# Kernel tuning notes

Hardware: AMD Instinct MI355X
Metric: run time of the kernel (lower is better)

## Reference

```python
import jax, jax.numpy as jnp
import numpy as np

W1 = 7          # half window
W2 = 2 * W1 + 1 # window size = 15
H = 4           # num heads
DH = 64         # head dim
DO = H * DH     # 256


def setup_inputs() -> dict:
    key = jax.random.key(0)
    ks = jax.random.split(key, 7)
    B, T, D = 2, 4096, 768
    s = 1.0 / np.sqrt(D).astype(np.float32)
    inputs = jax.random.normal(ks[0], (B, T, D), dtype=jnp.float32)
    Wq = jax.random.normal(ks[1], (DO, D), dtype=jnp.float32) * s
    bq = jax.random.normal(ks[2], (DO,), dtype=jnp.float32) * s
    Wv = jax.random.normal(ks[3], (DO, D), dtype=jnp.float32) * s
    bv = jax.random.normal(ks[4], (DO,), dtype=jnp.float32) * s
    pos_emb = jax.random.normal(ks[5], (W2, D), dtype=jnp.float32)
    return {"inputs": inputs, "Wq": Wq, "bq": bq, "Wv": Wv, "bv": bv, "pos_emb": pos_emb}


def reference(inputs, Wq, bq, Wv, bv, pos_emb):
    # Faithful to the torch module: k uses the *query* projection (source bug),
    # no softmax, no 1/sqrt(d) scaling.
    B, T, D = inputs.shape
    pad = jnp.pad(inputs, ((0, 0), (W1, W1), (0, 0)))  # [B, T+2*W1, D]
    # Project once on the padded sequence, then gather windows (linear ops
    # commute with the window gather; position bias added post-projection).
    q_pad = pad @ Wq.T + bq            # [B, T+2*W1, DO]
    v_pad = pad @ Wv.T + bv            # [B, T+2*W1, DO]
    pos_q = pos_emb @ Wq.T             # [W2, DO]  (query(window+pos) = query(window)+pos@Wq^T)
    pos_v = pos_emb @ Wv.T             # [W2, DO]
    idx = jnp.arange(T)[:, None] + jnp.arange(W2)[None, :]  # [T, W2]
    k = q_pad[:, idx] + pos_q          # [B, T, W2, DO]
    v = v_pad[:, idx] + pos_v          # [B, T, W2, DO]
    q = inputs @ Wq.T + bq             # [B, T, DO]
    qh = q.reshape(B, T, H, DH)
    kh = k.reshape(B, T, W2, H, DH)
    vh = v.reshape(B, T, W2, H, DH)
    scores = jnp.einsum('bthd,btwhd->bthw', qh, kh)   # [B, T, H, W2] (no softmax)
    ctx = jnp.einsum('bthw,btwhd->bthd', scores, vh)  # [B, T, H, DH]
    return ctx.reshape(B, T, DO)
```

## Files before the change

### kernel.cpp

```cpp
#include <hip/hip_runtime.h>

#define TPC   4110
#define MROWS 8220
#define MTOT  8235
#define MPAD  8320
#define KD    768
#define NSTR  4

typedef __attribute__((ext_vector_type(8))) short short8;
typedef __attribute__((ext_vector_type(4))) float f32x4;

#define LOAD_LDS16(gp, lp)                                                   \
  __builtin_amdgcn_global_load_lds(                                          \
      (const __attribute__((address_space(1))) void*)(gp),                   \
      (__attribute__((address_space(3))) void*)(lp), 16, 0, 0)

__device__ inline unsigned bfr(float x) {
  unsigned u = __float_as_uint(x);
  return (u + 0x7FFFu + ((u >> 16) & 1u)) >> 16;
}
__device__ inline unsigned pack2(float a, float b) {
  return bfr(a) | (bfr(b) << 16);
}

__global__ __launch_bounds__(256) void cast_pass(
    const float* __restrict__ inp, const float* __restrict__ Wq,
    const float* __restrict__ Wv, const float* __restrict__ pos,
    ushort* __restrict__ Abf, ushort* __restrict__ Wbf) {
  const int ACH = MPAD * 96;
  int gid = blockIdx.x * 256 + threadIdx.x;
  const float* src = nullptr;
  ushort* dst;
  if (gid < ACH) {
    int row = gid / 96, c = (gid - row * 96) * 8;
    dst = Abf + (size_t)row * KD + c;
    if (row < MROWS) {
      int b = row / TPC, tp = row - b * TPC, t = tp - 7;
      if (t >= 0 && t < 4096) src = inp + ((size_t)b * 4096 + t) * KD + c;
    } else if (row < MTOT) {
      src = pos + (size_t)(row - MROWS) * KD + c;
    }
  } else {
    int wid = gid - ACH;
    if (wid >= 512 * 96) return;
    int row = wid / 96, c = (wid - row * 96) * 8;
    dst = Wbf + (size_t)row * KD + c;
    src = (row < 256) ? Wq + (size_t)row * KD + c
                      : Wv + (size_t)(row - 256) * KD + c;
  }
  uint4 o;
  if (src) {
    float4 f0 = *(const float4*)src;
    float4 f1 = *(const float4*)(src + 4);
    o.x = pack2(f0.x, f0.y); o.y = pack2(f0.z, f0.w);
    o.z = pack2(f1.x, f1.y); o.w = pack2(f1.z, f1.w);
  } else {
    o.x = o.y = o.z = o.w = 0u;
  }
  *(uint4*)dst = o;
}

__global__ __launch_bounds__(256) void proj_gemm_bf16(
    const ushort* __restrict__ Abf, const ushort* __restrict__ Wbf,
    const float* __restrict__ bq, const float* __restrict__ bv,
    float* __restrict__ q_out, float* __restrict__ v_out) {
  __shared__ ushort Alds[128 * 32];
  __shared__ ushort Blds[128 * 32];
  const int tid = threadIdx.x;
  const int wave = tid >> 6, lane = tid & 63;
  const int nstrip = blockIdx.x;
  const int m0 = blockIdx.y * 128;
  const int wm = wave & 1, wn = wave >> 1;
  const int fr = lane & 15, quad = lane >> 4;

  f32x4 acc[4][4];
  #pragma unroll
  for (int i = 0; i < 4; i++)
    #pragma unroll
    for (int j = 0; j < 4; j++) acc[i][j] = 0.0f;

  const int r0 = tid >> 2, g0 = (tid & 3) * 8;
  const size_t a_base0 = (size_t)(m0 + r0) * KD + g0;
  const size_t a_base1 = (size_t)(m0 + 64 + r0) * KD + g0;
  const size_t b_base0 = (size_t)(nstrip * 128 + r0) * KD + g0;
  const size_t b_base1 = (size_t)(nstrip * 128 + 64 + r0) * KD + g0;
  ushort* aw0 = Alds + (size_t)(wave * 64) * 8;
  ushort* aw1 = Alds + (size_t)(256 + wave * 64) * 8;
  ushort* bw0 = Blds + (size_t)(wave * 64) * 8;
  ushort* bw1 = Blds + (size_t)(256 + wave * 64) * 8;

  for (int k0 = 0; k0 < KD; k0 += 32) {
    LOAD_LDS16(Abf + a_base0 + k0, aw0);
    LOAD_LDS16(Abf + a_base1 + k0, aw1);
    LOAD_LDS16(Wbf + b_base0 + k0, bw0);
    LOAD_LDS16(Wbf + b_base1 + k0, bw1);
    __syncthreads();
    short8 a[4], b[4];
    #pragma unroll
    for (int i = 0; i < 4; i++)
      a[i] = *(const short8*)(Alds + (wm * 64 + i * 16 + fr) * 32 + quad * 8);
    #pragma unroll
    for (int j = 0; j < 4; j++)
      b[j] = *(const short8*)(Blds + (wn * 64 + j * 16 + fr) * 32 + quad * 8);
    #pragma unroll
    for (int i = 0; i < 4; i++)
      #pragma unroll
      for (int j = 0; j < 4; j++)
        acc[i][j] = __builtin_amdgcn_mfma_f32_16x16x32_bf16(a[i], b[j],
                                                            acc[i][j], 0, 0, 0);
    __syncthreads();
  }

  const float* bias = (nstrip < 2) ? bq : bv;
  float* dst = (nstrip < 2) ? q_out : v_out;
  const int colb = (nstrip & 1) * 128;
  #pragma unroll
  for (int j = 0; j < 4; j++) {
    int col = colb + wn * 64 + j * 16 + fr;
    float bj = bias[col];
    #pragma unroll
    for (int i = 0; i < 4; i++) {
      int mbase = m0 + wm * 64 + i * 16 + quad * 4;
      #pragma unroll
      for (int r = 0; r < 4; r++) {
        int m = mbase + r;
        if (m < MTOT) {
          float v = acc[i][j][r] + (m < MROWS ? bj : 0.0f);
          dst[(size_t)m * 256 + col] = v;
        }
      }
    }
  }
}

__global__ __launch_bounds__(256) void win_attn2(
    const float* __restrict__ q_out, const float* __restrict__ v_out,
    float* __restrict__ out) {
  __shared__ __align__(16) float ks[78][68];
  __shared__ __align__(16) float vs[78][68];
  __shared__ __align__(16) float pq[15][68];
  __shared__ __align__(16) float pv[15][68];
  const int tid = threadIdx.x;
  const int bh = blockIdx.x >> 6, tile = blockIdx.x & 63;
  const int b = bh >> 2, h = bh & 3;
  const int t0 = tile * 64;
  const int colbase = h * 64;

  for (int idx = tid; idx < 78 * 16; idx += 256) {
    int row = idx >> 4, c4 = (idx & 15) * 4;
    size_t go = ((size_t)(b * TPC + t0 + row)) * 256 + colbase + c4;
    *(float4*)&ks[row][c4] = *(const float4*)(q_out + go);
    *(float4*)&vs[row][c4] = *(const float4*)(v_out + go);
  }
  if (tid < 15 * 16) {
    int row = tid >> 4, c4 = (tid & 15) * 4;
    size_t go = ((size_t)(MROWS + row)) * 256 + colbase + c4;
    *(float4*)&pq[row][c4] = *(const float4*)(q_out + go);
    *(float4*)&pv[row][c4] = *(const float4*)(v_out + go);
  }
  __syncthreads();

  const int tl = tid >> 2, qtr = tid & 3, d0 = qtr * 16;
  float4 qv[4];
  #pragma unroll
  for (int c = 0; c < 4; c++) qv[c] = *(float4*)&ks[tl + 7][d0 + c * 4];
  float4 ctx[4];
  #pragma unroll
  for (int c = 0; c < 4; c++) ctx[c] = make_float4(0.f, 0.f, 0.f, 0.f);

  #pragma unroll
  for (int w = 0; w < 15; w++) {
    float p = 0.f;
    #pragma unroll
    for (int c = 0; c < 4; c++) {
      float4 kk = *(float4*)&ks[tl + w][d0 + c * 4];
      float4 pp = *(float4*)&pq[w][d0 + c * 4];
      p += qv[c].x * (kk.x + pp.x) + qv[c].y * (kk.y + pp.y) +
           qv[c].z * (kk.z + pp.z) + qv[c].w * (kk.w + pp.w);
    }
    p += __shfl_xor(p, 1, 64);
    p += __shfl_xor(p, 2, 64);
    #pragma unroll
    for (int c = 0; c < 4; c++) {
      float4 vv = *(float4*)&vs[tl + w][d0 + c * 4];
      float4 pp = *(float4*)&pv[w][d0 + c * 4];
      ctx[c].x += p * (vv.x + pp.x);
      ctx[c].y += p * (vv.y + pp.y);
      ctx[c].z += p * (vv.z + pp.z);
      ctx[c].w += p * (vv.w + pp.w);
    }
  }
  size_t oo = ((size_t)(b * 4096 + t0 + tl)) * 256 + colbase + d0;
  #pragma unroll
  for (int c = 0; c < 4; c++) *(float4*)(out + oo + c * 4) = ctx[c];
}

extern "C" void kernel_launch(void* const* d_in, const int* in_sizes, int n_in,
                              void* d_out, int out_size, void* d_ws,
                              size_t ws_size, hipStream_t stream) {
  const float* inp = (const float*)d_in[0];
  const float* Wq  = (const float*)d_in[1];
  const float* bq  = (const float*)d_in[2];
  const float* Wv  = (const float*)d_in[3];
  const float* bv  = (const float*)d_in[4];
  const float* pos = (const float*)d_in[5];
  float* out = (float*)d_out;

  char* ws = (char*)d_ws;
  ushort* Abf  = (ushort*)ws;
  ushort* Wbf  = (ushort*)(ws + 12779520);
  float*  q_out = (float*)(ws + 13565952);
  float*  v_out = (float*)(ws + 22085632);

  const int cast_chunks = MPAD * 96 + 512 * 96;
  hipLaunchKernelGGL(cast_pass, dim3(cast_chunks / 256), dim3(256), 0, stream,
                     inp, Wq, Wv, pos, Abf, Wbf);
  hipLaunchKernelGGL(proj_gemm_bf16, dim3(NSTR, MPAD / 128), dim3(256), 0,
                     stream, Abf, Wbf, bq, bv, q_out, v_out);
  hipLaunchKernelGGL(win_attn2, dim3(2 * 4 * 64), dim3(256), 0, stream,
                     q_out, v_out, out);
}
```

Baseline: 119.5 us.

## Fuse bf16 cast into projection GEMM and store head-major Q/V slabs

Removes the separate cast kernel. The projection GEMM now loads fp32 inputs and weights directly, converts them to bf16 in registers and stores them to LDS, prefetching the next K tile into registers. The M tile shrinks from 128 to 64 with an occupancy hint, and Q/V outputs are written in a [b,h,t,d] layout with the position projections in separate buffers, so the attention kernel reads contiguous slabs. This trades the intermediate bf16 round trip and one launch for double the fp32 weight reads (redundant across M tiles), scattered epilogue stores, and register-staged loads instead of direct-to-LDS loads.

```diff
diff --git a/kernel.cpp b/kernel.cpp
--- a/kernel.cpp
+++ b/kernel.cpp
@@ -3,17 +3,10 @@
 #define TPC   4110
 #define MROWS 8220
 #define MTOT  8235
-#define MPAD  8320
 #define KD    768
-#define NSTR  4
 
 typedef __attribute__((ext_vector_type(8))) short short8;
 typedef __attribute__((ext_vector_type(4))) float f32x4;
-
-#define LOAD_LDS16(gp, lp)                                                   \
-  __builtin_amdgcn_global_load_lds(                                          \
-      (const __attribute__((address_space(1))) void*)(gp),                   \
-      (__attribute__((address_space(3))) void*)(lp), 16, 0, 0)
 
 __device__ inline unsigned bfr(float x) {
   unsigned u = __float_as_uint(x);
@@ -23,118 +16,123 @@
   return bfr(a) | (bfr(b) << 16);
 }
 
-__global__ __launch_bounds__(256) void cast_pass(
+__global__ __launch_bounds__(256, 3) void proj_fused(
     const float* __restrict__ inp, const float* __restrict__ Wq,
-    const float* __restrict__ Wv, const float* __restrict__ pos,
-    ushort* __restrict__ Abf, ushort* __restrict__ Wbf) {
-  const int ACH = MPAD * 96;
-  int gid = blockIdx.x * 256 + threadIdx.x;
-  const float* src = nullptr;
-  ushort* dst;
-  if (gid < ACH) {
-    int row = gid / 96, c = (gid - row * 96) * 8;
-    dst = Abf + (size_t)row * KD + c;
-    if (row < MROWS) {
-      int b = row / TPC, tp = row - b * TPC, t = tp - 7;
-      if (t >= 0 && t < 4096) src = inp + ((size_t)b * 4096 + t) * KD + c;
-    } else if (row < MTOT) {
-      src = pos + (size_t)(row - MROWS) * KD + c;
-    }
-  } else {
-    int wid = gid - ACH;
-    if (wid >= 512 * 96) return;
-    int row = wid / 96, c = (wid - row * 96) * 8;
-    dst = Wbf + (size_t)row * KD + c;
-    src = (row < 256) ? Wq + (size_t)row * KD + c
-                      : Wv + (size_t)(row - 256) * KD + c;
-  }
-  uint4 o;
-  if (src) {
-    float4 f0 = *(const float4*)src;
-    float4 f1 = *(const float4*)(src + 4);
-    o.x = pack2(f0.x, f0.y); o.y = pack2(f0.z, f0.w);
-    o.z = pack2(f1.x, f1.y); o.w = pack2(f1.z, f1.w);
-  } else {
-    o.x = o.y = o.z = o.w = 0u;
-  }
-  *(uint4*)dst = o;
-}
-
-__global__ __launch_bounds__(256) void proj_gemm_bf16(
-    const ushort* __restrict__ Abf, const ushort* __restrict__ Wbf,
-    const float* __restrict__ bq, const float* __restrict__ bv,
-    float* __restrict__ q_out, float* __restrict__ v_out) {
-  __shared__ ushort Alds[128 * 32];
-  __shared__ ushort Blds[128 * 32];
+    const float* __restrict__ bq, const float* __restrict__ Wv,
+    const float* __restrict__ bv, const float* __restrict__ pos,
+    float* __restrict__ q_out, float* __restrict__ v_out,
+    float* __restrict__ pos_q, float* __restrict__ pos_v) {
+  __shared__ ushort Al[64 * 32];
+  __shared__ ushort Bl[128 * 32];
   const int tid = threadIdx.x;
   const int wave = tid >> 6, lane = tid & 63;
-  const int nstrip = blockIdx.x;
-  const int m0 = blockIdx.y * 128;
+  const int ns = blockIdx.x;
+  const int m0 = blockIdx.y * 64;
   const int wm = wave & 1, wn = wave >> 1;
   const int fr = lane & 15, quad = lane >> 4;
 
-  f32x4 acc[4][4];
-  #pragma unroll
-  for (int i = 0; i < 4; i++)
+  const int sr = tid >> 2;
+  const int kc = (tid & 3) * 8;
+
+  const int am = m0 + sr;
+  const float* aptr = nullptr;
+  if (am < MROWS) {
+    int b = am / TPC, t = am - b * TPC - 7;
+    if (t >= 0 && t < 4096) aptr = inp + ((size_t)b * 4096 + t) * KD + kc;
+  } else if (am < MTOT) {
+    aptr = pos + (size_t)(am - MROWS) * KD + kc;
+  }
+  const float* wsrc = (ns < 2) ? Wq : Wv;
+  const int wbase = (ns & 1) * 128;
+  const float* bptr0 = wsrc + (size_t)(wbase + sr) * KD + kc;
+  const float* bptr1 = wsrc + (size_t)(wbase + 64 + sr) * KD + kc;
+
+  ushort* adst  = Al + sr * 32 + kc;
+  ushort* bdst0 = Bl + sr * 32 + kc;
+  ushort* bdst1 = Bl + (64 + sr) * 32 + kc;
+
+  f32x4 acc[2][4];
+  #pragma unroll
+  for (int i = 0; i < 2; i++)
     #pragma unroll
     for (int j = 0; j < 4; j++) acc[i][j] = 0.0f;
 
-  const int r0 = tid >> 2, g0 = (tid & 3) * 8;
-  const size_t a_base0 = (size_t)(m0 + r0) * KD + g0;
-  const size_t a_base1 = (size_t)(m0 + 64 + r0) * KD + g0;
-  const size_t b_base0 = (size_t)(nstrip * 128 + r0) * KD + g0;
-  const size_t b_base1 = (size_t)(nstrip * 128 + 64 + r0) * KD + g0;
-  ushort* aw0 = Alds + (size_t)(wave * 64) * 8;
-  ushort* aw1 = Alds + (size_t)(256 + wave * 64) * 8;
-  ushort* bw0 = Blds + (size_t)(wave * 64) * 8;
-  ushort* bw1 = Blds + (size_t)(256 + wave * 64) * 8;
+  float4 ra0, ra1, rb00, rb01, rb10, rb11;
+  if (aptr) { ra0 = *(const float4*)(aptr); ra1 = *(const float4*)(aptr + 4); }
+  else      { ra0 = ra1 = make_float4(0.f, 0.f, 0.f, 0.f); }
+  rb00 = *(const float4*)(bptr0); rb01 = *(const float4*)(bptr0 + 4);
+  rb10 = *(const float4*)(bptr1); rb11 = *(const float4*)(bptr1 + 4);
 
   for (int k0 = 0; k0 < KD; k0 += 32) {
-    LOAD_LDS16(Abf + a_base0 + k0, aw0);
-    LOAD_LDS16(Abf + a_base1 + k0, aw1);
-    LOAD_LDS16(Wbf + b_base0 + k0, bw0);
-    LOAD_LDS16(Wbf + b_base1 + k0, bw1);
+    uint4 o;
+    o.x = pack2(ra0.x, ra0.y); o.y = pack2(ra0.z, ra0.w);
+    o.z = pack2(ra1.x, ra1.y); o.w = pack2(ra1.z, ra1.w);
+    *(uint4*)adst = o;
+    o.x = pack2(rb00.x, rb00.y); o.y = pack2(rb00.z, rb00.w);
+    o.z = pack2(rb01.x, rb01.y); o.w = pack2(rb01.z, rb01.w);
+    *(uint4*)bdst0 = o;
+    o.x = pack2(rb10.x, rb10.y); o.y = pack2(rb10.z, rb10.w);
+    o.z = pack2(rb11.x, rb11.y); o.w = pack2(rb11.z, rb11.w);
+    *(uint4*)bdst1 = o;
+
+    float4 na0, na1, nb00, nb01, nb10, nb11;
+    const bool more = (k0 + 32 < KD);
+    if (more) {
+      int kn = k0 + 32;
+      if (aptr) { na0 = *(const float4*)(aptr + kn); na1 = *(const float4*)(aptr + kn + 4); }
+      else      { na0 = na1 = make_float4(0.f, 0.f, 0.f, 0.f); }
+      nb00 = *(const float4*)(bptr0 + kn); nb01 = *(const float4*)(bptr0 + kn + 4);
+      nb10 = *(const float4*)(bptr1 + kn); nb11 = *(const float4*)(bptr1 + kn + 4);
+    }
     __syncthreads();
-    short8 a[4], b[4];
-    #pragma unroll
-    for (int i = 0; i < 4; i++)
-      a[i] = *(const short8*)(Alds + (wm * 64 + i * 16 + fr) * 32 + quad * 8);
+    short8 af[2], bf[4];
+    #pragma unroll
+    for (int i = 0; i < 2; i++)
+      af[i] = *(const short8*)(Al + (wm * 32 + i * 16 + fr) * 32 + quad * 8);
     #pragma unroll
     for (int j = 0; j < 4; j++)
-      b[j] = *(const short8*)(Blds + (wn * 64 + j * 16 + fr) * 32 + quad * 8);
-    #pragma unroll
-    for (int i = 0; i < 4; i++)
+      bf[j] = *(const short8*)(Bl + (wn * 64 + j * 16 + fr) * 32 + quad * 8);
+    #pragma unroll
+    for (int i = 0; i < 2; i++)
       #pragma unroll
       for (int j = 0; j < 4; j++)
-        acc[i][j] = __builtin_amdgcn_mfma_f32_16x16x32_bf16(a[i], b[j],
+        acc[i][j] = __builtin_amdgcn_mfma_f32_16x16x32_bf16(af[i], bf[j],
                                                             acc[i][j], 0, 0, 0);
     __syncthreads();
-  }
-
-  const float* bias = (nstrip < 2) ? bq : bv;
-  float* dst = (nstrip < 2) ? q_out : v_out;
-  const int colb = (nstrip & 1) * 128;
+    if (more) {
+      ra0 = na0; ra1 = na1;
+      rb00 = nb00; rb01 = nb01; rb10 = nb10; rb11 = nb11;
+    }
+  }
+
+  const float* bias = (ns < 2) ? bq : bv;
+  float* outp = (ns < 2) ? q_out : v_out;
+  float* posp = (ns < 2) ? pos_q : pos_v;
   #pragma unroll
   for (int j = 0; j < 4; j++) {
-    int col = colb + wn * 64 + j * 16 + fr;
-    float bj = bias[col];
-    #pragma unroll
-    for (int i = 0; i < 4; i++) {
-      int mbase = m0 + wm * 64 + i * 16 + quad * 4;
+    const int colq = wbase + wn * 64 + j * 16 + fr;
+    const int h = colq >> 6, d = colq & 63;
+    const float bj = bias[colq];
+    #pragma unroll
+    for (int i = 0; i < 2; i++) {
+      const int mb = m0 + wm * 32 + i * 16 + quad * 4;
       #pragma unroll
       for (int r = 0; r < 4; r++) {
-        int m = mbase + r;
-        if (m < MTOT) {
-          float v = acc[i][j][r] + (m < MROWS ? bj : 0.0f);
-          dst[(size_t)m * 256 + col] = v;
+        const int m = mb + r;
+        if (m < MROWS) {
+          int b = m / TPC, tp = m - b * TPC;
+          outp[(((size_t)(b * 4 + h)) * TPC + tp) * 64 + d] = acc[i][j][r] + bj;
+        } else if (m < MTOT) {
+          posp[(m - MROWS) * 256 + colq] = acc[i][j][r];
         }
       }
     }
   }
 }
 
-__global__ __launch_bounds__(256) void win_attn2(
+__global__ __launch_bounds__(256) void win_attn3(
     const float* __restrict__ q_out, const float* __restrict__ v_out,
+    const float* __restrict__ pos_q, const float* __restrict__ pos_v,
     float* __restrict__ out) {
   __shared__ __align__(16) float ks[78][68];
   __shared__ __align__(16) float vs[78][68];
@@ -144,19 +142,19 @@
   const int bh = blockIdx.x >> 6, tile = blockIdx.x & 63;
   const int b = bh >> 2, h = bh & 3;
   const int t0 = tile * 64;
-  const int colbase = h * 64;
-
+
+  const size_t slab = (((size_t)(b * 4 + h)) * TPC + t0) * 64;
+  const float4* kq4 = (const float4*)(q_out + slab);
+  const float4* vv4 = (const float4*)(v_out + slab);
   for (int idx = tid; idx < 78 * 16; idx += 256) {
     int row = idx >> 4, c4 = (idx & 15) * 4;
-    size_t go = ((size_t)(b * TPC + t0 + row)) * 256 + colbase + c4;
-    *(float4*)&ks[row][c4] = *(const float4*)(q_out + go);
-    *(float4*)&vs[row][c4] = *(const float4*)(v_out + go);
+    *(float4*)&ks[row][c4] = kq4[idx];
+    *(float4*)&vs[row][c4] = vv4[idx];
   }
   if (tid < 15 * 16) {
     int row = tid >> 4, c4 = (tid & 15) * 4;
-    size_t go = ((size_t)(MROWS + row)) * 256 + colbase + c4;
-    *(float4*)&pq[row][c4] = *(const float4*)(q_out + go);
-    *(float4*)&pv[row][c4] = *(const float4*)(v_out + go);
+    *(float4*)&pq[row][c4] = *(const float4*)(pos_q + row * 256 + h * 64 + c4);
+    *(float4*)&pv[row][c4] = *(const float4*)(pos_v + row * 256 + h * 64 + c4);
   }
   __syncthreads();
 
@@ -190,7 +188,7 @@
       ctx[c].w += p * (vv.w + pp.w);
     }
   }
-  size_t oo = ((size_t)(b * 4096 + t0 + tl)) * 256 + colbase + d0;
+  size_t oo = ((size_t)(b * 4096 + t0 + tl)) * 256 + h * 64 + d0;
   #pragma unroll
   for (int c = 0; c < 4; c++) *(float4*)(out + oo + c * 4) = ctx[c];
 }
@@ -207,16 +205,13 @@
   float* out = (float*)d_out;
 
   char* ws = (char*)d_ws;
-  ushort* Abf  = (ushort*)ws;
-  ushort* Wbf  = (ushort*)(ws + 12779520);
-  float*  q_out = (float*)(ws + 13565952);
-  float*  v_out = (float*)(ws + 22085632);
-
-  const int cast_chunks = MPAD * 96 + 512 * 96;
-  hipLaunchKernelGGL(cast_pass, dim3(cast_chunks / 256), dim3(256), 0, stream,
-                     inp, Wq, Wv, pos, Abf, Wbf);
-  hipLaunchKernelGGL(proj_gemm_bf16, dim3(NSTR, MPAD / 128), dim3(256), 0,
-                     stream, Abf, Wbf, bq, bv, q_out, v_out);
-  hipLaunchKernelGGL(win_attn2, dim3(2 * 4 * 64), dim3(256), 0, stream,
-                     q_out, v_out, out);
-}
+  float* q_out = (float*)ws;
+  float* v_out = (float*)(ws + 8417280);
+  float* pos_q = (float*)(ws + 16834560);
+  float* pos_v = (float*)(ws + 16849920);
+
+  hipLaunchKernelGGL(proj_fused, dim3(4, 130), dim3(256), 0, stream,
+                     inp, Wq, bq, Wv, bv, pos, q_out, v_out, pos_q, pos_v);
+  hipLaunchKernelGGL(win_attn3, dim3(2 * 4 * 64), dim3(256), 0, stream,
+                     q_out, v_out, pos_q, pos_v, out);
+}
```

Measured after the change: 116.0 us. 2.9% less time.

## Store projections as bf16 in head-major layout and halve GEMM M-tile

Applied to the files above, without the earlier changes.

The projection GEMM now writes q/v as bf16 instead of fp32, in a per-(batch, head) contiguous layout, and writes the position projections to separate small buffers. The attention kernel reads contiguous bf16 slabs and widens them to fp32 in LDS. The GEMM M tile shrinks from 128 to 64 rows, doubling the block count for better occupancy across CUs. Together these cut intermediate memory traffic and improve load coalescing, at the cost of an extra bf16 rounding of q/k/v and scattered stores in the GEMM epilogue.

```diff
diff --git a/kernel.cpp b/kernel.cpp
--- a/kernel.cpp
+++ b/kernel.cpp
@@ -5,7 +5,6 @@
 #define MTOT  8235
 #define MPAD  8320
 #define KD    768
-#define NSTR  4
 
 typedef __attribute__((ext_vector_type(8))) short short8;
 typedef __attribute__((ext_vector_type(4))) float f32x4;
@@ -22,8 +21,10 @@
 __device__ inline unsigned pack2(float a, float b) {
   return bfr(a) | (bfr(b) << 16);
 }
-
-__global__ __launch_bounds__(256) void cast_pass(
+__device__ inline float bflo(unsigned u) { return __uint_as_float(u << 16); }
+__device__ inline float bfhi(unsigned u) { return __uint_as_float(u & 0xffff0000u); }
+
+__global__ __launch_bounds__(256) void cast_ab(
     const float* __restrict__ inp, const float* __restrict__ Wq,
     const float* __restrict__ Wv, const float* __restrict__ pos,
     ushort* __restrict__ Abf, ushort* __restrict__ Wbf) {
@@ -35,7 +36,7 @@
     int row = gid / 96, c = (gid - row * 96) * 8;
     dst = Abf + (size_t)row * KD + c;
     if (row < MROWS) {
-      int b = row / TPC, tp = row - b * TPC, t = tp - 7;
+      int b = row / TPC, t = row - b * TPC - 7;
       if (t >= 0 && t < 4096) src = inp + ((size_t)b * 4096 + t) * KD + c;
     } else if (row < MTOT) {
       src = pos + (size_t)(row - MROWS) * KD + c;
@@ -60,81 +61,85 @@
   *(uint4*)dst = o;
 }
 
-__global__ __launch_bounds__(256) void proj_gemm_bf16(
+__global__ __launch_bounds__(256) void gemm_bf16(
     const ushort* __restrict__ Abf, const ushort* __restrict__ Wbf,
     const float* __restrict__ bq, const float* __restrict__ bv,
-    float* __restrict__ q_out, float* __restrict__ v_out) {
-  __shared__ ushort Alds[128 * 32];
-  __shared__ ushort Blds[128 * 32];
+    ushort* __restrict__ q_out, ushort* __restrict__ v_out,
+    ushort* __restrict__ pos_q, ushort* __restrict__ pos_v) {
+  __shared__ ushort Al[64 * 32];
+  __shared__ ushort Bl[128 * 32];
   const int tid = threadIdx.x;
   const int wave = tid >> 6, lane = tid & 63;
-  const int nstrip = blockIdx.x;
-  const int m0 = blockIdx.y * 128;
+  const int ns = blockIdx.x;
+  const int m0 = blockIdx.y * 64;
   const int wm = wave & 1, wn = wave >> 1;
   const int fr = lane & 15, quad = lane >> 4;
 
-  f32x4 acc[4][4];
-  #pragma unroll
-  for (int i = 0; i < 4; i++)
+  const int srow = tid >> 2, skc = (tid & 3) * 8;
+  const ushort* ag  = Abf + (size_t)(m0 + srow) * KD + skc;
+  const ushort* bg0 = Wbf + (size_t)(ns * 128 + srow) * KD + skc;
+  const ushort* bg1 = bg0 + (size_t)64 * KD;
+  ushort* al  = Al + wave * 512;
+  ushort* bl0 = Bl + wave * 512;
+  ushort* bl1 = Bl + 2048 + wave * 512;
+
+  f32x4 acc[2][4];
+  #pragma unroll
+  for (int i = 0; i < 2; i++)
     #pragma unroll
     for (int j = 0; j < 4; j++) acc[i][j] = 0.0f;
 
-  const int r0 = tid >> 2, g0 = (tid & 3) * 8;
-  const size_t a_base0 = (size_t)(m0 + r0) * KD + g0;
-  const size_t a_base1 = (size_t)(m0 + 64 + r0) * KD + g0;
-  const size_t b_base0 = (size_t)(nstrip * 128 + r0) * KD + g0;
-  const size_t b_base1 = (size_t)(nstrip * 128 + 64 + r0) * KD + g0;
-  ushort* aw0 = Alds + (size_t)(wave * 64) * 8;
-  ushort* aw1 = Alds + (size_t)(256 + wave * 64) * 8;
-  ushort* bw0 = Blds + (size_t)(wave * 64) * 8;
-  ushort* bw1 = Blds + (size_t)(256 + wave * 64) * 8;
-
   for (int k0 = 0; k0 < KD; k0 += 32) {
-    LOAD_LDS16(Abf + a_base0 + k0, aw0);
-    LOAD_LDS16(Abf + a_base1 + k0, aw1);
-    LOAD_LDS16(Wbf + b_base0 + k0, bw0);
-    LOAD_LDS16(Wbf + b_base1 + k0, bw1);
+    LOAD_LDS16(ag + k0, al);
+    LOAD_LDS16(bg0 + k0, bl0);
+    LOAD_LDS16(bg1 + k0, bl1);
     __syncthreads();
-    short8 a[4], b[4];
-    #pragma unroll
-    for (int i = 0; i < 4; i++)
-      a[i] = *(const short8*)(Alds + (wm * 64 + i * 16 + fr) * 32 + quad * 8);
+    short8 af[2], bf[4];
+    #pragma unroll
+    for (int i = 0; i < 2; i++)
+      af[i] = *(const short8*)(Al + (wm * 32 + i * 16 + fr) * 32 + quad * 8);
     #pragma unroll
     for (int j = 0; j < 4; j++)
-      b[j] = *(const short8*)(Blds + (wn * 64 + j * 16 + fr) * 32 + quad * 8);
-    #pragma unroll
-    for (int i = 0; i < 4; i++)
+      bf[j] = *(const short8*)(Bl + (wn * 64 + j * 16 + fr) * 32 + quad * 8);
+    #pragma unroll
+    for (int i = 0; i < 2; i++)
       #pragma unroll
       for (int j = 0; j < 4; j++)
-        acc[i][j] = __builtin_amdgcn_mfma_f32_16x16x32_bf16(a[i], b[j],
+        acc[i][j] = __builtin_amdgcn_mfma_f32_16x16x32_bf16(af[i], bf[j],
                                                             acc[i][j], 0, 0, 0);
     __syncthreads();
   }
 
-  const float* bias = (nstrip < 2) ? bq : bv;
-  float* dst = (nstrip < 2) ? q_out : v_out;
-  const int colb = (nstrip & 1) * 128;
+  const float* bias = (ns < 2) ? bq : bv;
+  ushort* outp = (ns < 2) ? q_out : v_out;
+  ushort* posp = (ns < 2) ? pos_q : pos_v;
+  const int wbase = (ns & 1) * 128;
   #pragma unroll
   for (int j = 0; j < 4; j++) {
-    int col = colb + wn * 64 + j * 16 + fr;
-    float bj = bias[col];
-    #pragma unroll
-    for (int i = 0; i < 4; i++) {
-      int mbase = m0 + wm * 64 + i * 16 + quad * 4;
+    const int colq = wbase + wn * 64 + j * 16 + fr;
+    const int h = colq >> 6, d = colq & 63;
+    const float bj = bias[colq];
+    #pragma unroll
+    for (int i = 0; i < 2; i++) {
+      const int mb = m0 + wm * 32 + i * 16 + quad * 4;
       #pragma unroll
       for (int r = 0; r < 4; r++) {
-        int m = mbase + r;
-        if (m < MTOT) {
-          float v = acc[i][j][r] + (m < MROWS ? bj : 0.0f);
-          dst[(size_t)m * 256 + col] = v;
+        const int m = mb + r;
+        if (m < MROWS) {
+          int b = m / TPC, tp = m - b * TPC;
+          outp[(((size_t)(b * 4 + h)) * TPC + tp) * 64 + d] =
+              (ushort)bfr(acc[i][j][r] + bj);
+        } else if (m < MTOT) {
+          posp[(m - MROWS) * 256 + colq] = (ushort)bfr(acc[i][j][r]);
         }
       }
     }
   }
 }
 
-__global__ __launch_bounds__(256) void win_attn2(
-    const float* __restrict__ q_out, const float* __restrict__ v_out,
+__global__ __launch_bounds__(256) void win_attn4(
+    const ushort* __restrict__ q_out, const ushort* __restrict__ v_out,
+    const ushort* __restrict__ pos_q, const ushort* __restrict__ pos_v,
     float* __restrict__ out) {
   __shared__ __align__(16) float ks[78][68];
   __shared__ __align__(16) float vs[78][68];
@@ -144,19 +149,33 @@
   const int bh = blockIdx.x >> 6, tile = blockIdx.x & 63;
   const int b = bh >> 2, h = bh & 3;
   const int t0 = tile * 64;
-  const int colbase = h * 64;
-
-  for (int idx = tid; idx < 78 * 16; idx += 256) {
-    int row = idx >> 4, c4 = (idx & 15) * 4;
-    size_t go = ((size_t)(b * TPC + t0 + row)) * 256 + colbase + c4;
-    *(float4*)&ks[row][c4] = *(const float4*)(q_out + go);
-    *(float4*)&vs[row][c4] = *(const float4*)(v_out + go);
-  }
-  if (tid < 15 * 16) {
-    int row = tid >> 4, c4 = (tid & 15) * 4;
-    size_t go = ((size_t)(MROWS + row)) * 256 + colbase + c4;
-    *(float4*)&pq[row][c4] = *(const float4*)(q_out + go);
-    *(float4*)&pv[row][c4] = *(const float4*)(v_out + go);
+
+  const size_t slab = (((size_t)(b * 4 + h)) * TPC + t0) * 64;
+  for (int idx = tid; idx < 624; idx += 256) {
+    int row = idx >> 3, c8 = (idx & 7) * 8;
+    uint4 kc = *(const uint4*)(q_out + slab + idx * 8);
+    ks[row][c8 + 0] = bflo(kc.x); ks[row][c8 + 1] = bfhi(kc.x);
+    ks[row][c8 + 2] = bflo(kc.y); ks[row][c8 + 3] = bfhi(kc.y);
+    ks[row][c8 + 4] = bflo(kc.z); ks[row][c8 + 5] = bfhi(kc.z);
+    ks[row][c8 + 6] = bflo(kc.w); ks[row][c8 + 7] = bfhi(kc.w);
+    uint4 vc = *(const uint4*)(v_out + slab + idx * 8);
+    vs[row][c8 + 0] = bflo(vc.x); vs[row][c8 + 1] = bfhi(vc.x);
+    vs[row][c8 + 2] = bflo(vc.y); vs[row][c8 + 3] = bfhi(vc.y);
+    vs[row][c8 + 4] = bflo(vc.z); vs[row][c8 + 5] = bfhi(vc.z);
+    vs[row][c8 + 6] = bflo(vc.w); vs[row][c8 + 7] = bfhi(vc.w);
+  }
+  if (tid < 120) {
+    int row = tid >> 3, c8 = (tid & 7) * 8;
+    uint4 qc = *(const uint4*)(pos_q + row * 256 + h * 64 + c8);
+    pq[row][c8 + 0] = bflo(qc.x); pq[row][c8 + 1] = bfhi(qc.x);
+    pq[row][c8 + 2] = bflo(qc.y); pq[row][c8 + 3] = bfhi(qc.y);
+    pq[row][c8 + 4] = bflo(qc.z); pq[row][c8 + 5] = bfhi(qc.z);
+    pq[row][c8 + 6] = bflo(qc.w); pq[row][c8 + 7] = bfhi(qc.w);
+    uint4 vc = *(const uint4*)(pos_v + row * 256 + h * 64 + c8);
+    pv[row][c8 + 0] = bflo(vc.x); pv[row][c8 + 1] = bfhi(vc.x);
+    pv[row][c8 + 2] = bflo(vc.y); pv[row][c8 + 3] = bfhi(vc.y);
+    pv[row][c8 + 4] = bflo(vc.z); pv[row][c8 + 5] = bfhi(vc.z);
+    pv[row][c8 + 6] = bflo(vc.w); pv[row][c8 + 7] = bfhi(vc.w);
   }
   __syncthreads();
 
@@ -190,7 +209,7 @@
       ctx[c].w += p * (vv.w + pp.w);
     }
   }
-  size_t oo = ((size_t)(b * 4096 + t0 + tl)) * 256 + colbase + d0;
+  size_t oo = ((size_t)(b * 4096 + t0 + tl)) * 256 + h * 64 + d0;
   #pragma unroll
   for (int c = 0; c < 4; c++) *(float4*)(out + oo + c * 4) = ctx[c];
 }
@@ -207,16 +226,18 @@
   float* out = (float*)d_out;
 
   char* ws = (char*)d_ws;
-  ushort* Abf  = (ushort*)ws;
-  ushort* Wbf  = (ushort*)(ws + 12779520);
-  float*  q_out = (float*)(ws + 13565952);
-  float*  v_out = (float*)(ws + 22085632);
+  ushort* Abf   = (ushort*)ws;
+  ushort* Wbf   = (ushort*)(ws + 12779520);
+  ushort* q_out = (ushort*)(ws + 13565952);
+  ushort* v_out = (ushort*)(ws + 17774592);
+  ushort* pos_q = (ushort*)(ws + 21983232);
+  ushort* pos_v = (ushort*)(ws + 21990912);
 
   const int cast_chunks = MPAD * 96 + 512 * 96;
-  hipLaunchKernelGGL(cast_pass, dim3(cast_chunks / 256), dim3(256), 0, stream,
+  hipLaunchKernelGGL(cast_ab, dim3(cast_chunks / 256), dim3(256), 0, stream,
                      inp, Wq, Wv, pos, Abf, Wbf);
-  hipLaunchKernelGGL(proj_gemm_bf16, dim3(NSTR, MPAD / 128), dim3(256), 0,
-                     stream, Abf, Wbf, bq, bv, q_out, v_out);
-  hipLaunchKernelGGL(win_attn2, dim3(2 * 4 * 64), dim3(256), 0, stream,
-                     q_out, v_out, out);
-}
+  hipLaunchKernelGGL(gemm_bf16, dim3(4, MPAD / 64), dim3(256), 0, stream,
+                     Abf, Wbf, bq, bv, q_out, v_out, pos_q, pos_v);
+  hipLaunchKernelGGL(win_attn4, dim3(2 * 4 * 64), dim3(256), 0, stream,
+                     q_out, v_out, pos_q, pos_v, out);
+}
```

New measurement: 113.1 us. -5.3%, faster.
